# Kernel optimization log

Measured on AMD Instinct MI355X. Metric: run time of the kernel, lower is better.

## Reference

```python
import jax, jax.numpy as jnp
import numpy as np

NUM_HEADS = 16

def setup_inputs() -> dict:
    key = jax.random.key(0)
    ks = jax.random.split(key, 5)
    d_model = 1024
    x = jax.random.normal(ks[0], (2, 2048, d_model), dtype=jnp.float32)
    # xavier-uniform-like scale for square [d_model, d_model] weights
    lim = float(np.sqrt(6.0 / (d_model + d_model)))
    def w(k):
        return jax.random.uniform(k, (d_model, d_model), dtype=jnp.float32, minval=-lim, maxval=lim)
    return {"x": x, "Wq": w(ks[1]), "Wk": w(ks[2]), "Wv": w(ks[3]), "Wo": w(ks[4])}

def reference(x, Wq, Wk, Wv, Wo):
    B, S, D = x.shape
    H = NUM_HEADS
    dk = D // H
    # project: torch does x @ W.T
    def split_heads(t):
        return t.reshape(B, S, H, dk).transpose(0, 2, 1, 3)  # [B,H,S,dk]
    q = split_heads(x @ Wq.T)
    k = split_heads(x @ Wk.T)
    v = split_heads(x @ Wv.T)
    scores = jnp.einsum('bhqd,bhkd->bhqk', q, k) / jnp.sqrt(jnp.float32(dk))
    causal = jnp.tril(jnp.ones((S, S), dtype=bool))  # True where attended
    scores = jnp.where(causal[None, None], scores, -jnp.inf)
    probs = jax.nn.softmax(scores, axis=-1)
    out = jnp.einsum('bhqk,bhkd->bhqd', probs, v)  # [B,H,S,dk]
    out = out.transpose(0, 2, 1, 3).reshape(B, S, D)
    return out @ Wo.T
```

## Files before the change

### kernel.cpp

```cpp
#include <hip/hip_runtime.h>
#include <stdint.h>

#define BATCH  2
#define SEQ    2048
#define DMODEL 1024
#define NHEADS 16
#define DKH    64
#define MTOT   (BATCH*SEQ)
#define VSTR   (SEQ + 32)

typedef unsigned short u16;
typedef __bf16 bf16x8 __attribute__((ext_vector_type(8)));
typedef float  f32x4  __attribute__((ext_vector_type(4)));

extern "C" __device__ float __ocml_native_exp2_f32(float);

__device__ __forceinline__ u16 f2bf(float f) {
  union { float f; uint32_t u; } v; v.f = f;
  uint32_t u = v.u;
  return (u16)((u + 0x7FFFu + ((u >> 16) & 1u)) >> 16);
}
__device__ __forceinline__ float bf2f(u16 h) {
  union { uint32_t u; float f; } v; v.u = (uint32_t)h << 16; return v.f;
}

__device__ __forceinline__ void gld_lds16(const void* g, void* l) {
  __builtin_amdgcn_global_load_lds(
      (__attribute__((address_space(1))) void*)g,
      (__attribute__((address_space(3))) void*)l, 16, 0, 0);
}

__device__ __forceinline__ uint32_t cvtpk(float lo, float hi) {
  uint32_t r;
  asm("v_cvt_pk_bf16_f32 %0, %1, %2" : "=v"(r) : "v"(lo), "v"(hi));
  return r;
}
__device__ __forceinline__ void pl16swap(uint32_t& a, uint32_t& b) {
  asm volatile("v_permlane16_swap_b32 %0, %1" : "+v"(a), "+v"(b));
}

__global__ void cvt_f32_bf16(const float* __restrict__ src, u16* __restrict__ dst) {
  size_t i = ((size_t)blockIdx.x * 256 + threadIdx.x) * 4;
  float4 f = *(const float4*)(src + i);
  ushort4 o;
  o.x = f2bf(f.x); o.y = f2bf(f.y); o.z = f2bf(f.z); o.w = f2bf(f.w);
  *(ushort4*)(dst + i) = o;
}
__global__ void cvt_w(const float* __restrict__ a, const float* __restrict__ b,
                      const float* __restrict__ c, const float* __restrict__ d,
                      u16* __restrict__ dst) {
  const float* srcs[4] = {a, b, c, d};
  const float* s = srcs[blockIdx.y];
  size_t i = ((size_t)blockIdx.x * 256 + threadIdx.x) * 4;
  float4 f = *(const float4*)(s + i);
  ushort4 o;
  o.x = f2bf(f.x); o.y = f2bf(f.y); o.z = f2bf(f.z); o.w = f2bf(f.w);
  *(ushort4*)(dst + (size_t)blockIdx.y * (DMODEL*DMODEL) + i) = o;
}

__global__ __launch_bounds__(256, 3) void gemm_qkv(
    const u16* __restrict__ xb, const u16* __restrict__ wq,
    const u16* __restrict__ wk, const u16* __restrict__ wv,
    u16* __restrict__ q, u16* __restrict__ k, u16* __restrict__ v, float qscale) {
  __shared__ __align__(16) u16 lA[128 * 64];
  __shared__ __align__(16) u16 lB[3][64 * 64];

  const int tid  = threadIdx.x;
  const int lane = tid & 63;
  const int lrow = lane & 15;
  const int quad = lane >> 4;
  const int wave = tid >> 6;
  const int wm   = (wave & 1) * 64;
  const int wn   = (wave >> 1) * 32;
  const int sx   = lrow & 7;
  const int m0 = blockIdx.x * 128, n0 = blockIdx.y * 64;
  const u16* Ws[3] = {wq, wk, wv};

  f32x4 acc[3][4][2] = {};

  for (int k0 = 0; k0 < DMODEL; k0 += 64) {
    #pragma unroll
    for (int r = 0; r < 4; ++r) {
      int off  = r * 4096 + tid * 16;
      int row  = off >> 7;
      int c16  = (off >> 4) & 7;
      int colb = (c16 ^ (row & 7)) << 4;
      gld_lds16((const char*)xb + ((size_t)(m0 + row) * DMODEL + k0) * 2 + colb,
                (char*)lA + off);
    }
    #pragma unroll
    for (int z = 0; z < 3; ++z)
      #pragma unroll
      for (int r = 0; r < 2; ++r) {
        int off  = r * 4096 + tid * 16;
        int row  = off >> 7;
        int c16  = (off >> 4) & 7;
        int colb = (c16 ^ (row & 7)) << 4;
        gld_lds16((const char*)Ws[z] + ((size_t)(n0 + row) * DMODEL + k0) * 2 + colb,
                  (char*)&lB[z][0] + off);
      }
    __syncthreads();
    #pragma unroll
    for (int ks = 0; ks < 2; ++ks) {
      const int ro = ((((ks << 2) | quad) ^ sx) << 3);
      bf16x8 a[4], b[3][2];
      #pragma unroll
      for (int i = 0; i < 4; ++i)
        a[i] = *(const bf16x8*)(lA + (wm + i*16 + lrow) * 64 + ro);
      #pragma unroll
      for (int z = 0; z < 3; ++z)
        #pragma unroll
        for (int j = 0; j < 2; ++j)
          b[z][j] = *(const bf16x8*)(&lB[z][0] + (wn + j*16 + lrow) * 64 + ro);
      #pragma unroll
      for (int z = 0; z < 3; ++z)
        #pragma unroll
        for (int i = 0; i < 4; ++i)
          #pragma unroll
          for (int j = 0; j < 2; ++j)
            acc[z][i][j] = __builtin_amdgcn_mfma_f32_16x16x32_bf16(a[i], b[z][j], acc[z][i][j], 0, 0, 0);
    }
    __syncthreads();
  }

  const int rb = quad * 4, cb = lrow;
  const int h  = blockIdx.y;
  u16* outs[3] = {q, k, v};
  #pragma unroll
  for (int z = 0; z < 3; ++z) {
    u16* out = outs[z];
    if (z == 2) {
      #pragma unroll
      for (int i = 0; i < 4; ++i)
        #pragma unroll
        for (int j = 0; j < 2; ++j) {
          int row0 = m0 + wm + i*16 + rb;
          int d_   = wn + j*16 + cb;
          int b_ = row0 >> 11, s0 = row0 & 2047;
          ushort4 pk;
          pk.x = f2bf(acc[z][i][j][0]); pk.y = f2bf(acc[z][i][j][1]);
          pk.z = f2bf(acc[z][i][j][2]); pk.w = f2bf(acc[z][i][j][3]);
          *(ushort4*)&out[((size_t)(b_*NHEADS + h) * DKH + d_) * VSTR + s0] = pk;
        }
    } else {
      const float scale = (z == 0) ? qscale : 1.0f;
      #pragma unroll
      for (int i = 0; i < 4; ++i)
        #pragma unroll
        for (int j = 0; j < 2; ++j)
          #pragma unroll
          for (int r = 0; r < 4; ++r) {
            int row = m0 + wm + i*16 + rb + r;
            int d_  = wn + j*16 + cb;
            int b_ = row >> 11, s_ = row & 2047;
            out[(((size_t)(b_*NHEADS + h) * SEQ + s_) << 6) + d_] =
                f2bf(acc[z][i][j][r] * scale);
          }
    }
  }
}

__device__ __forceinline__ void gemm_core64(const u16* A, const u16* W,
                                            int m0, int n0, f32x4 acc[4][2],
                                            u16* lA, u16* lB) {
  const int tid  = threadIdx.x;
  const int lane = tid & 63;
  const int lrow = lane & 15;
  const int quad = lane >> 4;
  const int wave = tid >> 6;
  const int wm   = (wave & 1) * 64;
  const int wn   = (wave >> 1) * 32;
  const int sx   = lrow & 7;

  for (int k0 = 0; k0 < DMODEL; k0 += 64) {
    #pragma unroll
    for (int r = 0; r < 4; ++r) {
      int off  = r * 4096 + tid * 16;
      int row  = off >> 7;
      int c16  = (off >> 4) & 7;
      int colb = (c16 ^ (row & 7)) << 4;
      gld_lds16((const char*)A + ((size_t)(m0 + row) * DMODEL + k0) * 2 + colb,
                (char*)lA + off);
    }
    #pragma unroll
    for (int r = 0; r < 2; ++r) {
      int off  = r * 4096 + tid * 16;
      int row  = off >> 7;
      int c16  = (off >> 4) & 7;
      int colb = (c16 ^ (row & 7)) << 4;
      gld_lds16((const char*)W + ((size_t)(n0 + row) * DMODEL + k0) * 2 + colb,
                (char*)lB + off);
    }
    __syncthreads();
    #pragma unroll
    for (int ks = 0; ks < 2; ++ks) {
      bf16x8 a[4], b[2];
      const int ro = ((((ks << 2) | quad) ^ sx) << 3);
      #pragma unroll
      for (int i = 0; i < 4; ++i)
        a[i] = *(const bf16x8*)(lA + (wm + i*16 + lrow) * 64 + ro);
      #pragma unroll
      for (int j = 0; j < 2; ++j)
        b[j] = *(const bf16x8*)(lB + (wn + j*16 + lrow) * 64 + ro);
      #pragma unroll
      for (int i = 0; i < 4; ++i)
        #pragma unroll
        for (int j = 0; j < 2; ++j)
          acc[i][j] = __builtin_amdgcn_mfma_f32_16x16x32_bf16(a[i], b[j], acc[i][j], 0, 0, 0);
    }
    __syncthreads();
  }
}

__global__ __launch_bounds__(256, 3) void gemm_out(
    const u16* __restrict__ ab, const u16* __restrict__ wo, float* __restrict__ out) {
  __shared__ __align__(16) u16 lA[128 * 64];
  __shared__ __align__(16) u16 lB[64 * 64];
  const int m0 = blockIdx.x * 128, n0 = blockIdx.y * 64;
  f32x4 acc[4][2] = {};
  gemm_core64(ab, wo, m0, n0, acc, lA, lB);

  const int lane = threadIdx.x & 63;
  const int wave = threadIdx.x >> 6;
  const int wm = (wave & 1) * 64, wn = (wave >> 1) * 32;
  const int rb = (lane >> 4) * 4, cb = lane & 15;
  #pragma unroll
  for (int i = 0; i < 4; ++i)
    #pragma unroll
    for (int j = 0; j < 2; ++j)
      #pragma unroll
      for (int r = 0; r < 4; ++r)
        out[(size_t)(m0 + wm + i*16 + rb + r) * DMODEL + (n0 + wn + j*16 + cb)]
            = acc[i][j][r];
}

__device__ const uint8_t JT[40] = {
  60,61,62,63, 56,57,58, 52,53,54, 48,49,50, 44,45,46, 40,41, 36,37,
  32,33, 28,29, 24, 20, 16, 12,
  59,42,25,8, 55,38,21,4, 51,34,17,0
};

__device__ __forceinline__ void stage_kv(const u16* Kg, const u16* Vg, int t,
                                         u16* lK, u16* lV, int tid) {
  #pragma unroll
  for (int r = 0; r < 2; ++r) {
    int off  = r * 4096 + tid * 16;
    int row  = off >> 7;
    int colb = (((off >> 4) & 7) ^ (row & 7)) << 4;
    gld_lds16((const char*)Kg + ((size_t)(t*64 + row) * DKH) * 2 + colb,
              (char*)lK + off);
    gld_lds16((const char*)Vg + ((size_t)row * VSTR + t*64) * 2 + colb,
              (char*)lV + off);
  }
}

__global__ __launch_bounds__(256, 3) void attn(
    const u16* __restrict__ Q, const u16* __restrict__ K,
    const u16* __restrict__ V, u16* __restrict__ O,
    u16* __restrict__ po, float* __restrict__ pl) {
  __shared__ __align__(16) u16 lK[2][64 * 64];
  __shared__ __align__(16) u16 lV[2][64 * 64];

  const int tid  = threadIdx.x;
  const int wid  = tid >> 6;
  const int lane = tid & 63;
  const int lrow = lane & 15;
  const int quad = lane >> 4;
  const int sx   = lrow & 7;
  const int pq   = ((quad & 1) << 1) | (quad >> 1);

  const int g  = blockIdx.x >> 5;
  const int bh = blockIdx.x & 31;
  const int e  = JT[g];
  const int u  = e >> 2, c = e & 3;
  const int lo = c * 8;
  const int T  = 2*u + 2;
  const int hi = (lo + 8 < T) ? lo + 8 : T;
  const int td = 2*u + (wid >> 1);
  const int qg0 = 128*u + 32*wid;

  const u16* Qg = Q + (size_t)bh * SEQ * DKH;
  const u16* Kg = K + (size_t)bh * SEQ * DKH;
  const u16* Vg = V + (size_t)bh * DKH * VSTR;

  bf16x8 aq[2][2];
  #pragma unroll
  for (int i = 0; i < 2; ++i)
    #pragma unroll
    for (int ks = 0; ks < 2; ++ks)
      aq[i][ks] = *(const bf16x8*)(Qg + (size_t)(qg0 + 16*i + lrow) * DKH + ks*32 + quad*8);

  f32x4 o_acc[2][4] = {};
  float l_acc[2] = {};

  stage_kv(Kg, Vg, lo, &lK[0][0], &lV[0][0], tid);
  __syncthreads();
  int cur = 0;

  for (int t = lo; t < hi; ++t) {
    if (t + 1 < hi)
      stage_kv(Kg, Vg, t + 1, &lK[cur ^ 1][0], &lV[cur ^ 1][0], tid);

    f32x4 s_acc[2][4] = {};
    {
      bf16x8 kf[2][4];
      #pragma unroll
      for (int ks = 0; ks < 2; ++ks) {
        const int kro = ((((ks << 2) | quad) ^ sx) << 3);
        #pragma unroll
        for (int j = 0; j < 4; ++j)
          kf[ks][j] = *(const bf16x8*)(&lK[cur][0] + (j*16 + lrow) * 64 + kro);
      }
      __builtin_amdgcn_s_setprio(1);
      #pragma unroll
      for (int i = 0; i < 2; ++i)
        #pragma unroll
        for (int ks = 0; ks < 2; ++ks)
          #pragma unroll
          for (int j = 0; j < 4; ++j)
            s_acc[i][j] = __builtin_amdgcn_mfma_f32_16x16x32_bf16(kf[ks][j], aq[i][ks], s_acc[i][j], 0, 0, 0);
      __builtin_amdgcn_s_setprio(0);
    }

    bf16x8 vf[2][4];
    #pragma unroll
    for (int ks = 0; ks < 2; ++ks) {
      const int vro = ((((ks << 2) | pq) ^ sx) << 3);
      #pragma unroll
      for (int j = 0; j < 4; ++j)
        vf[ks][j] = *(const bf16x8*)(&lV[cur][0] + (j*16 + lrow) * 64 + vro);
    }

    #pragma unroll
    for (int i = 0; i < 2; ++i) {
      if (t >= td) {
        const int qrel = qg0 + 16*i + lrow - 64*t;
        #pragma unroll
        for (int j = 0; j < 4; ++j) {
          int kl = j*16 + quad*4;
          #pragma unroll
          for (int r = 0; r < 4; ++r)
            if (kl + r > qrel) s_acc[i][j][r] = -1e30f;
        }
      }

      uint32_t w[4][2];
      float ls = 0.f;
      #pragma unroll
      for (int j = 0; j < 4; ++j) {
        float p0 = __ocml_native_exp2_f32(s_acc[i][j][0]);
        float p1 = __ocml_native_exp2_f32(s_acc[i][j][1]);
        float p2 = __ocml_native_exp2_f32(s_acc[i][j][2]);
        float p3 = __ocml_native_exp2_f32(s_acc[i][j][3]);
        ls += (p0 + p1) + (p2 + p3);
        w[j][0] = cvtpk(p0, p1);
        w[j][1] = cvtpk(p2, p3);
      }
      l_acc[i] += ls;

      pl16swap(w[0][0], w[1][0]);
      pl16swap(w[0][1], w[1][1]);
      pl16swap(w[2][0], w[3][0]);
      pl16swap(w[2][1], w[3][1]);
      union { uint32_t u[4]; bf16x8 v; } g0, g1;
      g0.u[0] = w[0][0]; g0.u[1] = w[0][1]; g0.u[2] = w[1][0]; g0.u[3] = w[1][1];
      g1.u[0] = w[2][0]; g1.u[1] = w[2][1]; g1.u[2] = w[3][0]; g1.u[3] = w[3][1];

      __builtin_amdgcn_s_setprio(1);
      #pragma unroll
      for (int j = 0; j < 4; ++j)
        o_acc[i][j] = __builtin_amdgcn_mfma_f32_16x16x32_bf16(g0.v, vf[0][j], o_acc[i][j], 0, 0, 0);
      #pragma unroll
      for (int j = 0; j < 4; ++j)
        o_acc[i][j] = __builtin_amdgcn_mfma_f32_16x16x32_bf16(g1.v, vf[1][j], o_acc[i][j], 0, 0, 0);
      __builtin_amdgcn_s_setprio(0);
    }

    __syncthreads();
    cur ^= 1;
  }

  float lr[2][4];
  #pragma unroll
  for (int i = 0; i < 2; ++i) {
    float s = l_acc[i];
    s += __shfl_xor(s, 16, 64);
    s += __shfl_xor(s, 32, 64);
    #pragma unroll
    for (int r = 0; r < 4; ++r)
      lr[i][r] = __shfl(s, quad*4 + r, 16);
  }

  if (T <= 8) {
    const int h = bh & 15, b_ = bh >> 4;
    #pragma unroll
    for (int i = 0; i < 2; ++i)
      #pragma unroll
      for (int j = 0; j < 4; ++j)
        #pragma unroll
        for (int r = 0; r < 4; ++r) {
          int sg = qg0 + 16*i + quad*4 + r;
          O[(size_t)(b_ * SEQ + sg) * DMODEL + h * DKH + j*16 + lrow]
              = f2bf(o_acc[i][j][r] / lr[i][r]);
        }
  } else {
    const int pold = td;
    const int base = (pold < 16) ? (pold - 8) * 2
                   : (pold < 24) ? 16 + (pold - 16) * 3
                   :               40 + (pold - 24) * 4;
    const int slot = (base + c) * 32 + bh;
    const int r64  = 32 * (wid & 1);
    #pragma unroll
    for (int i = 0; i < 2; ++i) {
      #pragma unroll
      for (int j = 0; j < 4; ++j) {
        ushort4 pk;
        pk.x = f2bf(o_acc[i][j][0]); pk.y = f2bf(o_acc[i][j][1]);
        pk.z = f2bf(o_acc[i][j][2]); pk.w = f2bf(o_acc[i][j][3]);
        *(ushort4*)&po[(size_t)slot * 4096 + (j*16 + lrow) * 64 + r64 + 16*i + quad*4] = pk;
      }
      if (lrow == 0)
        #pragma unroll
        for (int r = 0; r < 4; ++r)
          pl[slot * 64 + r64 + 16*i + quad*4 + r] = lr[i][r];
    }
  }
}

__global__ __launch_bounds__(256) void combine(
    const u16* __restrict__ po, const float* __restrict__ pl, u16* __restrict__ ab) {
  __shared__ u16 Ls[64][68];
  const int b  = blockIdx.x;
  const int p  = 8 + (b >> 5);
  const int bh = b & 31;
  const int t  = threadIdx.x;
  const int col = t >> 2;
  const int r0  = (t & 3) * 16;
  const int base = (p < 16) ? (p - 8) * 2
                 : (p < 24) ? 16 + (p - 16) * 3
                 :            40 + (p - 24) * 4;
  const int nc   = (p < 16) ? 2 : (p < 24) ? 3 : 4;

  float acc[16], lsum[16];
  const size_t s0 = (size_t)(base * 32 + bh);
  const u16*   q0 = po + s0 * 4096 + col * 64 + r0;
  const float* l0 = pl + s0 * 64 + r0;
  #pragma unroll
  for (int q4 = 0; q4 < 4; ++q4) {
    ushort4 a  = *(const ushort4*)(q0 + q4 * 4);
    ushort4 c2 = *(const ushort4*)(q0 + (size_t)32 * 4096 + q4 * 4);
    acc[q4*4+0] = bf2f(a.x) + bf2f(c2.x);
    acc[q4*4+1] = bf2f(a.y) + bf2f(c2.y);
    acc[q4*4+2] = bf2f(a.z) + bf2f(c2.z);
    acc[q4*4+3] = bf2f(a.w) + bf2f(c2.w);
    float4 f = *(const float4*)(l0 + q4 * 4);
    float4 g = *(const float4*)(l0 + 32 * 64 + q4 * 4);
    lsum[q4*4+0] = f.x + g.x; lsum[q4*4+1] = f.y + g.y;
    lsum[q4*4+2] = f.z + g.z; lsum[q4*4+3] = f.w + g.w;
  }
  if (nc >= 3) {
    #pragma unroll
    for (int q4 = 0; q4 < 4; ++q4) {
      ushort4 a = *(const ushort4*)(q0 + (size_t)64 * 4096 + q4 * 4);
      acc[q4*4+0] += bf2f(a.x); acc[q4*4+1] += bf2f(a.y);
      acc[q4*4+2] += bf2f(a.z); acc[q4*4+3] += bf2f(a.w);
      float4 f = *(const float4*)(l0 + 64 * 64 + q4 * 4);
      lsum[q4*4+0] += f.x; lsum[q4*4+1] += f.y;
      lsum[q4*4+2] += f.z; lsum[q4*4+3] += f.w;
    }
  }
  if (nc == 4) {
    #pragma unroll
    for (int q4 = 0; q4 < 4; ++q4) {
      ushort4 a = *(const ushort4*)(q0 + (size_t)96 * 4096 + q4 * 4);
      acc[q4*4+0] += bf2f(a.x); acc[q4*4+1] += bf2f(a.y);
      acc[q4*4+2] += bf2f(a.z); acc[q4*4+3] += bf2f(a.w);
      float4 f = *(const float4*)(l0 + 96 * 64 + q4 * 4);
      lsum[q4*4+0] += f.x; lsum[q4*4+1] += f.y;
      lsum[q4*4+2] += f.z; lsum[q4*4+3] += f.w;
    }
  }
  #pragma unroll
  for (int q = 0; q < 16; ++q)
    Ls[r0 + q][col] = f2bf(acc[q] / lsum[q]);
  __syncthreads();

  const int row = t >> 2;
  const int c0  = (t & 3) * 16;
  const int b_ = bh >> 4, h = bh & 15;
  u16* dst = ab + (size_t)(b_ * SEQ + 64 * p + row) * DMODEL + h * DKH + c0;
  #pragma unroll
  for (int q = 0; q < 16; q += 4)
    *(ushort4*)(dst + q) = *(const ushort4*)&Ls[row][c0 + q];
}

extern "C" void kernel_launch(void* const* d_in, const int* in_sizes, int n_in,
                              void* d_out, int out_size, void* d_ws, size_t ws_size,
                              hipStream_t stream) {
  const float* x  = (const float*)d_in[0];
  const float* Wq = (const float*)d_in[1];
  const float* Wk = (const float*)d_in[2];
  const float* Wv = (const float*)d_in[3];
  const float* Wo = (const float*)d_in[4];
  float* out = (float*)d_out;

  u16* xb  = (u16*)d_ws;
  u16* wqb = xb  + (size_t)MTOT * DMODEL;
  u16* wkb = wqb + (size_t)DMODEL * DMODEL;
  u16* wvb = wkb + (size_t)DMODEL * DMODEL;
  u16* wob = wvb + (size_t)DMODEL * DMODEL;
  u16* qb  = wob + (size_t)DMODEL * DMODEL;
  u16* kb  = qb  + (size_t)MTOT * DMODEL;
  u16* vb  = kb  + (size_t)MTOT * DMODEL;
  u16* ab  = vb  + (size_t)BATCH * NHEADS * DKH * VSTR;
  u16* po  = ab  + (size_t)MTOT * DMODEL;
  float* pl = (float*)(po + (size_t)2304 * 4096);

  cvt_f32_bf16<<<MTOT * DMODEL / 1024, 256, 0, stream>>>(x, xb);
  cvt_w<<<dim3(DMODEL * DMODEL / 1024, 4), 256, 0, stream>>>(Wq, Wk, Wv, Wo, wqb);

  const float qscale = 0.125f * 1.44269504088896340736f;
  gemm_qkv<<<dim3(32, 16), 256, 0, stream>>>(
      xb, wqb, wkb, wvb, qb, kb, vb, qscale);

  attn<<<1280, 256, 0, stream>>>(qb, kb, vb, ab, po, pl);
  combine<<<768, 256, 0, stream>>>(po, pl, ab);

  gemm_out<<<dim3(32, 16), 256, 0, stream>>>(ab, wob, out);
}
```

Baseline: 163.1 us.

## Split causal attention KV range into finer 4-tile chunks with generalized combine

Changes the split-KV decomposition of causal attention from chunks of up to 8 KV tiles to chunks of up to 4. This raises the attention grid from 1280 to 2304 blocks to even out per-block work and fill the GPU better. The combine kernel is generalized with a prefix table and a loop over a variable number of partial chunks, and the partial-result workspace grows. The cost is more partial outputs written and read back, plus more combine work.

```diff
diff --git a/kernel.cpp b/kernel.cpp
--- a/kernel.cpp
+++ b/kernel.cpp
@@ -234,11 +234,25 @@
             = acc[i][j][r];
 }
 
-__device__ const uint8_t JT[40] = {
-  60,61,62,63, 56,57,58, 52,53,54, 48,49,50, 44,45,46, 40,41, 36,37,
-  32,33, 28,29, 24, 20, 16, 12,
-  59,42,25,8, 55,38,21,4, 51,34,17,0
+__device__ const uint8_t JT[72] = {
+  120,121,122,123,124,125,126,127,
+  112,113,114,115,116,117,118,
+  104,105,106,107,108,109,110,
+  96,97,98,99,100,101,
+  88,89,90,91,92,93,
+  80,81,82,83,84,
+  72,73,74,75,76,
+  64,65,66,67,
+  56,57,58,59,
+  48,49,50,
+  40,41,42,
+  32,33,
+  24,25,
+  16,
+  8,
+  119,102,85,68,51,34,17,0
 };
+__device__ const uint8_t PFX[16] = {0,0,0,4,8,14,20,28,36,46,56,68,80,94,108,124};
 
 __device__ __forceinline__ void stage_kv(const u16* Kg, const u16* Vg, int t,
                                          u16* lK, u16* lV, int tid) {
@@ -272,10 +286,10 @@
   const int g  = blockIdx.x >> 5;
   const int bh = blockIdx.x & 31;
   const int e  = JT[g];
-  const int u  = e >> 2, c = e & 3;
-  const int lo = c * 8;
+  const int u  = e >> 3, c = e & 7;
+  const int lo = c * 4;
   const int T  = 2*u + 2;
-  const int hi = (lo + 8 < T) ? lo + 8 : T;
+  const int hi = (lo + 4 < T) ? lo + 4 : T;
   const int td = 2*u + (wid >> 1);
   const int qg0 = 128*u + 32*wid;
 
@@ -391,7 +405,7 @@
       lr[i][r] = __shfl(s, quad*4 + r, 16);
   }
 
-  if (T <= 8) {
+  if (T <= 4) {
     const int h = bh & 15, b_ = bh >> 4;
     #pragma unroll
     for (int i = 0; i < 2; ++i)
@@ -405,10 +419,8 @@
         }
   } else {
     const int pold = td;
-    const int base = (pold < 16) ? (pold - 8) * 2
-                   : (pold < 24) ? 16 + (pold - 16) * 3
-                   :               40 + (pold - 24) * 4;
-    const int slot = (base + c) * 32 + bh;
+    const int nc   = (u + 2) >> 1;
+    const int slot = (PFX[u] + (pold & 1) * nc + c) * 32 + bh;
     const int r64  = 32 * (wid & 1);
     #pragma unroll
     for (int i = 0; i < 2; ++i) {
@@ -427,19 +439,20 @@
   }
 }
 
+__device__ const uint8_t PFXc[16] = {0,0,0,4,8,14,20,28,36,46,56,68,80,94,108,124};
+
 __global__ __launch_bounds__(256) void combine(
     const u16* __restrict__ po, const float* __restrict__ pl, u16* __restrict__ ab) {
   __shared__ u16 Ls[64][68];
   const int b  = blockIdx.x;
-  const int p  = 8 + (b >> 5);
+  const int p  = 4 + (b >> 5);
   const int bh = b & 31;
   const int t  = threadIdx.x;
   const int col = t >> 2;
   const int r0  = (t & 3) * 16;
-  const int base = (p < 16) ? (p - 8) * 2
-                 : (p < 24) ? 16 + (p - 16) * 3
-                 :            40 + (p - 24) * 4;
-  const int nc   = (p < 16) ? 2 : (p < 24) ? 3 : 4;
+  const int u    = p >> 1;
+  const int nc   = (u + 2) >> 1;
+  const int base = PFXc[u] + (p & 1) * nc;
 
   float acc[16], lsum[16];
   const size_t s0 = (size_t)(base * 32 + bh);
@@ -447,35 +460,20 @@
   const float* l0 = pl + s0 * 64 + r0;
   #pragma unroll
   for (int q4 = 0; q4 < 4; ++q4) {
-    ushort4 a  = *(const ushort4*)(q0 + q4 * 4);
-    ushort4 c2 = *(const ushort4*)(q0 + (size_t)32 * 4096 + q4 * 4);
-    acc[q4*4+0] = bf2f(a.x) + bf2f(c2.x);
-    acc[q4*4+1] = bf2f(a.y) + bf2f(c2.y);
-    acc[q4*4+2] = bf2f(a.z) + bf2f(c2.z);
-    acc[q4*4+3] = bf2f(a.w) + bf2f(c2.w);
+    ushort4 a = *(const ushort4*)(q0 + q4 * 4);
+    acc[q4*4+0] = bf2f(a.x); acc[q4*4+1] = bf2f(a.y);
+    acc[q4*4+2] = bf2f(a.z); acc[q4*4+3] = bf2f(a.w);
     float4 f = *(const float4*)(l0 + q4 * 4);
-    float4 g = *(const float4*)(l0 + 32 * 64 + q4 * 4);
-    lsum[q4*4+0] = f.x + g.x; lsum[q4*4+1] = f.y + g.y;
-    lsum[q4*4+2] = f.z + g.z; lsum[q4*4+3] = f.w + g.w;
-  }
-  if (nc >= 3) {
+    lsum[q4*4+0] = f.x; lsum[q4*4+1] = f.y;
+    lsum[q4*4+2] = f.z; lsum[q4*4+3] = f.w;
+  }
+  for (int ch = 1; ch < nc; ++ch) {
     #pragma unroll
     for (int q4 = 0; q4 < 4; ++q4) {
-      ushort4 a = *(const ushort4*)(q0 + (size_t)64 * 4096 + q4 * 4);
+      ushort4 a = *(const ushort4*)(q0 + (size_t)ch * 32 * 4096 + q4 * 4);
       acc[q4*4+0] += bf2f(a.x); acc[q4*4+1] += bf2f(a.y);
       acc[q4*4+2] += bf2f(a.z); acc[q4*4+3] += bf2f(a.w);
-      float4 f = *(const float4*)(l0 + 64 * 64 + q4 * 4);
-      lsum[q4*4+0] += f.x; lsum[q4*4+1] += f.y;
-      lsum[q4*4+2] += f.z; lsum[q4*4+3] += f.w;
-    }
-  }
-  if (nc == 4) {
-    #pragma unroll
-    for (int q4 = 0; q4 < 4; ++q4) {
-      ushort4 a = *(const ushort4*)(q0 + (size_t)96 * 4096 + q4 * 4);
-      acc[q4*4+0] += bf2f(a.x); acc[q4*4+1] += bf2f(a.y);
-      acc[q4*4+2] += bf2f(a.z); acc[q4*4+3] += bf2f(a.w);
-      float4 f = *(const float4*)(l0 + 96 * 64 + q4 * 4);
+      float4 f = *(const float4*)(l0 + (size_t)ch * 32 * 64 + q4 * 4);
       lsum[q4*4+0] += f.x; lsum[q4*4+1] += f.y;
       lsum[q4*4+2] += f.z; lsum[q4*4+3] += f.w;
     }
@@ -514,7 +512,7 @@
   u16* vb  = kb  + (size_t)MTOT * DMODEL;
   u16* ab  = vb  + (size_t)BATCH * NHEADS * DKH * VSTR;
   u16* po  = ab  + (size_t)MTOT * DMODEL;
-  float* pl = (float*)(po + (size_t)2304 * 4096);
+  float* pl = (float*)(po + (size_t)4480 * 4096);
 
   cvt_f32_bf16<<<MTOT * DMODEL / 1024, 256, 0, stream>>>(x, xb);
   cvt_w<<<dim3(DMODEL * DMODEL / 1024, 4), 256, 0, stream>>>(Wq, Wk, Wv, Wo, wqb);
@@ -523,8 +521,8 @@
   gemm_qkv<<<dim3(32, 16), 256, 0, stream>>>(
       xb, wqb, wkb, wvb, qb, kb, vb, qscale);
 
-  attn<<<1280, 256, 0, stream>>>(qb, kb, vb, ab, po, pl);
-  combine<<<768, 256, 0, stream>>>(po, pl, ab);
+  attn<<<2304, 256, 0, stream>>>(qb, kb, vb, ab, po, pl);
+  combine<<<896, 256, 0, stream>>>(po, pl, ab);
 
   gemm_out<<<dim3(32, 16), 256, 0, stream>>>(ab, wob, out);
 }
```

New measurement: 169.7 us. 1.04x slower.
